# Kernel optimization log

Hardware: AMD Instinct MI355X
Metric: run time of the kernel (lower is better)

## Reference

```python
import jax, jax.numpy as jnp
import numpy as np

B, F, S = 2, 512, 1024
E = 4
I = 1024          # intermediate = 2 * features
K = 3             # conv kernel size
INIT_SCALE = 1.0
EPS = 1e-5
SLOPE = 0.02


def setup_inputs() -> dict:
    key = jax.random.key(0)
    k = jax.random.split(key, 6)
    inp = jax.random.normal(k[0], (B, F, S), jnp.float32)
    divisor = (jnp.arange(S, dtype=jnp.float32) + 1.0).reshape(1, 1, S)
    w0_gate = jax.random.normal(k[1], (E, F, 1), jnp.float32) * (F ** -0.5)
    w0 = jax.random.normal(k[2], (E, F, 3 * I), jnp.float32) * (F ** -0.5)
    w1 = jax.random.normal(k[3], (3 * I, I, K), jnp.float32) * ((I * K) ** -0.5)
    w2_gate = jax.random.normal(k[4], (E, I, 1), jnp.float32) * (I ** -0.5)
    w2 = jax.random.normal(k[5], (E, I, F), jnp.float32) * (I ** -0.5)
    return {"inp": inp, "divisor": divisor, "w0_gate": w0_gate, "w0": w0,
            "w1": w1, "w2_gate": w2_gate, "w2": w2}


def _norm(x):
    # channel norm over dim 1: subtract mean, divide by scaled L2 norm
    x = x - jnp.mean(x, axis=1, keepdims=True)
    n = jnp.sqrt(jnp.sum(x * x, axis=1, keepdims=True)) * (x.shape[1] ** -0.5)
    return x / (n + EPS)


def _moe(x, gate, w):
    # x: [B,F,S]; gate: [E,F,1]; w: [E,F,D]
    logits = jnp.einsum('bfs,ef->bes', x, gate[:, :, 0])          # [B,E,S]
    gates = jax.nn.softmax(logits, axis=1)
    idx = jnp.argmax(logits, axis=1)                              # [B,S]
    one_hot = jax.nn.one_hot(idx, w.shape[0], dtype=x.dtype)      # [B,S,E]
    # straight-through gumbel-style gate: hard one-hot fwd, soft grad
    gumbel = jnp.transpose(one_hot, (0, 2, 1)) - jax.lax.stop_gradient(gates) + gates  # [B,E,S]
    xs = jnp.transpose(x, (0, 2, 1))                              # [B,S,F]
    out = jnp.zeros((x.shape[0], x.shape[2], w.shape[2]), x.dtype)
    for e in range(w.shape[0]):  # small fixed expert count
        mask = one_hot[:, :, e][:, :, None]                       # [B,S,1]
        out = out + mask * ((xs * gumbel[:, e, :, None]) @ w[e])
    loss = jnp.sum(jnp.mean(gates, axis=(0, 2)) * jnp.mean(one_hot, axis=(0, 1)))
    return loss, jnp.transpose(out, (0, 2, 1))                    # [B,D,S]


def _conv1d(x, w, causal_pad):
    if causal_pad and w.shape[-1] > 1:
        x = jnp.pad(x, ((0, 0), (0, 0), (w.shape[-1] - 1, 0)))
    return jax.lax.conv_general_dilated(
        x, w, window_strides=(1,), padding='VALID',
        dimension_numbers=('NCH', 'OIH', 'NCH'), feature_group_count=1)


def reference(inp, divisor, w0_gate, w0, w1, w2_gate, w2):
    loss0, h = _moe(inp, w0_gate, w0)                 # [B,3I,S]
    depth, scale, shift = jnp.split(h, 3, axis=1)     # each [B,I,S]
    cum = jnp.cumsum(depth, axis=-1)
    h = jax.nn.leaky_relu(_norm(cum / divisor * scale + shift), SLOPE)
    h = _conv1d(h, w1, causal_pad=True)               # [B,3I,S]
    s0, s1, sh = jnp.split(h, 3, axis=1)
    h = jax.nn.leaky_relu(_norm(s0 * s1 + sh), SLOPE)
    loss1, out = _moe(h, w2_gate, w2)                 # [B,F,S]
    return out * INIT_SCALE, loss0 + loss1
```

## Files before the change

kernel.cpp:

```cpp
#include <hip/hip_runtime.h>
#include <hip/hip_bf16.h>

#define SDIM 1024

typedef float f32x4 __attribute__((ext_vector_type(4)));
typedef short short8 __attribute__((ext_vector_type(8)));

__device__ __forceinline__ unsigned short f2bf(float f) {
    __hip_bfloat16 h = __float2bfloat16(f);
    return *reinterpret_cast<unsigned short*>(&h);
}
__device__ __forceinline__ float bf2f(unsigned short u) {
    return __uint_as_float(((unsigned int)u) << 16);
}
__device__ __forceinline__ void gload_lds16(const unsigned short* g, unsigned short* l) {
    __builtin_amdgcn_global_load_lds((const __attribute__((address_space(1))) void*)g,
                                     (__attribute__((address_space(3))) void*)l, 16, 0, 0);
}

__device__ __forceinline__ void tr_split(
    const float* __restrict__ in, unsigned short* __restrict__ oh,
    unsigned short* __restrict__ ol, int R, int C, size_t sliceStride,
    int bx, int by, int slice, int tid, float (*t)[33])
{
    int c0 = bx * 32, r0 = by * 32;
    int cc = tid & 31, r8 = tid >> 5;
    const float* ip = in + slice * sliceStride;
    #pragma unroll
    for (int k = 0; k < 4; ++k) {
        int r = r8 + k * 8;
        t[r][cc] = ip[(size_t)(r0 + r) * C + c0 + cc];
    }
    __syncthreads();
    #pragma unroll
    for (int k = 0; k < 4; ++k) {
        int rr = r8 + k * 8;
        float v = t[cc][rr];
        unsigned short hi = f2bf(v);
        unsigned short lo = f2bf(v - bf2f(hi));
        size_t o = slice * sliceStride + (size_t)(c0 + rr) * R + r0 + cc;
        oh[o] = hi; ol[o] = lo;
    }
}

__global__ __launch_bounds__(256) void prep_kernel(
    const float* __restrict__ inp, const float* __restrict__ w0,
    const float* __restrict__ w1,
    unsigned short* __restrict__ xTh, unsigned short* __restrict__ xTl,
    unsigned short* __restrict__ w0Th, unsigned short* __restrict__ w0Tl,
    unsigned short* __restrict__ w1Th, unsigned short* __restrict__ w1Tl,
    const float* __restrict__ wg, int* __restrict__ idx, float* __restrict__ acc)
{
    __shared__ float t[32][33];
    __shared__ float wgs[4 * 512];
    __shared__ float part[32][4][9];
    __shared__ float la[8];
    int id = blockIdx.x;
    int tid = threadIdx.x;
    if (id < 1024) {
        int bx = id & 31, by = (id >> 5) & 15, slice = id >> 9;
        tr_split(inp, xTh, xTl, 512, 1024, (size_t)512 * 1024, bx, by, slice, tid, t);
    } else if (id < 7168) {
        int m = id - 1024;
        int bx = m % 96, by = (m / 96) & 15, slice = m / 1536;
        tr_split(w0, w0Th, w0Tl, 512, 3072, (size_t)512 * 3072, bx, by, slice, tid, t);
    } else if (id < 19456) {
        int tt = (id - 7168) * 256 + tid;
        int o = tt >> 10, i = tt & 1023;
        const float* p = w1 + (size_t)o * 3072 + i * 3;
        #pragma unroll
        for (int k = 0; k < 3; ++k) {
            float v = p[k];
            unsigned short hi = f2bf(v);
            unsigned short lo = f2bf(v - bf2f(hi));
            size_t off = (size_t)k * 3145728 + (size_t)o * 1024 + i;
            w1Th[off] = hi; w1Tl[off] = lo;
        }
    } else {
        if (tid < 8) la[tid] = 0.f;
        for (int l = tid; l < 2048; l += 256) wgs[l] = wg[l];
        __syncthreads();
        int t0 = (id - 19456) * 8;
        int b = t0 >> 10, s0 = t0 & 1023;
        int sl = tid & 7, fg = tid >> 3;
        float l0 = 0.f, l1 = 0.f, l2 = 0.f, l3 = 0.f;
        for (int f = fg; f < 512; f += 32) {
            float xv = inp[((size_t)b * 512 + f) * SDIM + s0 + sl];
            l0 += xv * wgs[f];
            l1 += xv * wgs[512 + f];
            l2 += xv * wgs[1024 + f];
            l3 += xv * wgs[1536 + f];
        }
        part[fg][0][sl] = l0; part[fg][1][sl] = l1;
        part[fg][2][sl] = l2; part[fg][3][sl] = l3;
        __syncthreads();
        for (int h = 16; h >= 1; h >>= 1) {
            if (fg < h) {
                #pragma unroll
                for (int e = 0; e < 4; ++e) part[fg][e][sl] += part[fg + h][e][sl];
            }
            __syncthreads();
        }
        if (fg == 0) {
            float L[4] = {part[0][0][sl], part[0][1][sl], part[0][2][sl], part[0][3][sl]};
            float m = fmaxf(fmaxf(L[0], L[1]), fmaxf(L[2], L[3]));
            float e0 = expf(L[0] - m), e1 = expf(L[1] - m), e2 = expf(L[2] - m), e3 = expf(L[3] - m);
            float inv = 1.0f / (e0 + e1 + e2 + e3);
            int best = 0; float bv = L[0];
            if (L[1] > bv) { bv = L[1]; best = 1; }
            if (L[2] > bv) { bv = L[2]; best = 2; }
            if (L[3] > bv) { bv = L[3]; best = 3; }
            idx[t0 + sl] = best;
            atomicAdd(&la[0], e0 * inv);
            atomicAdd(&la[1], e1 * inv);
            atomicAdd(&la[2], e2 * inv);
            atomicAdd(&la[3], e3 * inv);
            atomicAdd(&la[4 + best], 1.0f);
        }
        __syncthreads();
        if (tid < 8) atomicAdd(&acc[tid], la[tid]);
    }
}

__global__ __launch_bounds__(1024) void sort_kernel(
    const int* __restrict__ idx, int* __restrict__ perm, int* __restrict__ eSorted)
{
    int b = blockIdx.x;
    int tid = threadIdx.x;
    int lane = tid & 63, w = tid >> 6;
    int e = idx[(b << 10) + tid];
    __shared__ int wcnt[16][4];
    __shared__ int woff[16][4];
    int r = 0;
    unsigned long long lt = (1ull << lane) - 1ull;
    #pragma unroll
    for (int eo = 0; eo < 4; ++eo) {
        unsigned long long m = __ballot(e == eo);
        if (lane == 0) wcnt[w][eo] = __popcll(m);
        if (e == eo) r = __popcll(m & lt);
    }
    __syncthreads();
    if (tid == 0) {
        int baseAcc = 0;
        for (int eo = 0; eo < 4; ++eo)
            for (int ww = 0; ww < 16; ++ww) { woff[ww][eo] = baseAcc; baseAcc += wcnt[ww][eo]; }
    }
    __syncthreads();
    int pos = woff[w][e] + r;
    perm[(b << 10) + pos] = tid;
    eSorted[(b << 10) + pos] = e;
}

__global__ __launch_bounds__(768) void moe_split_kernel(
    const unsigned short* __restrict__ base, unsigned int XH, unsigned int XL,
    unsigned int WH, unsigned int WL,
    const int* __restrict__ perm, const int* __restrict__ eSorted,
    float* __restrict__ out)
{
    extern __shared__ unsigned short lds[];
    const int BUF = 40960;
    int id = blockIdx.x;
    int wg = (id & 7) * 32 + (id >> 3);
    int t0 = (wg & 7) * 256;
    int d0 = (wg >> 3) * 96;
    int b = t0 >> 10, s0 = t0 & 1023;
    int tid = threadIdx.x;
    int lane = tid & 63;
    int lm = lane & 15, q = lane >> 4;
    int wid = tid >> 6;
    int wm = (wid >> 2) * 32, wn = (wid & 3) * 64;

    int eLo = eSorted[(b << 10) + s0];
    int eHi = eSorted[(b << 10) + s0 + 255];

    unsigned int gofs[7];
    int lofs[7], doSeg[7];
    #pragma unroll
    for (int j = 0; j < 7; ++j) {
        int seg = wid + 12 * j;
        gofs[j] = 0; lofs[j] = 0; doSeg[j] = 0;
        if (seg < 80) {
            int row = seg * 16 + (lane >> 2);
            int slot = lane & 3;
            int c = slot ^ ((row >> 1) & 3);
            unsigned int src;
            int act = 1;
            if (row < 512) {
                int gr = (row < 256) ? row : row - 256;
                unsigned int hb = (row < 256) ? XH : XL;
                int tj = perm[(b << 10) + s0 + gr];
                src = hb + (unsigned int)(((b << 10) + tj) * 512) + c * 8;
            } else {
                int R = row - 512;
                unsigned int hb = WH;
                if (R >= 384) { R -= 384; hb = WL; }
                int e = R / 96, dl = R - e * 96;
                act = (e >= eLo && e <= eHi) ? 1 : 0;
                src = hb + (unsigned int)((e * 3072 + d0 + dl) * 512) + c * 8;
            }
            gofs[j] = src;
            lofs[j] = seg * 512 + lane * 8;
            doSeg[j] = act;
        }
    }

    int bofH[4];
    #pragma unroll
    for (int fn = 0; fn < 4; ++fn) {
        int row = wn + fn * 16 + lm;
        bofH[fn] = row * 32 + ((q ^ ((row >> 1) & 3)) << 3);
    }
    int aofH[4][2];
    #pragma unroll
    for (int e = 0; e < 4; ++e)
        #pragma unroll
        for (int fm = 0; fm < 2; ++fm) {
            int row = 512 + e * 96 + wm + fm * 16 + lm;
            aofH[e][fm] = row * 32 + ((q ^ ((row >> 1) & 3)) << 3);
        }

    int eidx[4], sv[4];
    #pragma unroll
    for (int fn = 0; fn < 4; ++fn) {
        int sl = (b << 10) + s0 + wn + fn * 16 + lm;
        eidx[fn] = eSorted[sl];
        sv[fn]   = perm[sl];
    }
    bool presF[4][4], presE[4];
    #pragma unroll
    for (int e = 0; e < 4; ++e) {
        presE[e] = false;
        #pragma unroll
        for (int fn = 0; fn < 4; ++fn) {
            presF[e][fn] = __any(eidx[fn] == e);
            presE[e] = presE[e] || presF[e][fn];
        }
    }

    f32x4 acc[2][4];
    #pragma unroll
    for (int fm = 0; fm < 2; ++fm)
        #pragma unroll
        for (int fn = 0; fn < 4; ++fn)
            acc[fm][fn] = (f32x4){0.f, 0.f, 0.f, 0.f};

    const short8 z = {0, 0, 0, 0, 0, 0, 0, 0};

    #pragma unroll
    for (int j = 0; j < 7; ++j)
        if (doSeg[j]) gload_lds16(base + gofs[j], lds + lofs[j]);

    int curOfs = 0;
    for (int f0 = 0; f0 < 512; f0 += 32) {
        __syncthreads();
        int nxtOfs = curOfs ^ BUF;
        if (f0 + 32 < 512) {
            #pragma unroll
            for (int j = 0; j < 7; ++j)
                if (doSeg[j]) gload_lds16(base + gofs[j] + f0 + 32, lds + nxtOfs + lofs[j]);
        }

        const unsigned short* lb = lds + curOfs;
        short8 bh[4], bl[4];
        #pragma unroll
        for (int fn = 0; fn < 4; ++fn) {
            bh[fn] = *(const short8*)(lb + bofH[fn]);
            bl[fn] = *(const short8*)(lb + bofH[fn] + 8192);
        }
        #pragma unroll
        for (int e = 0; e < 4; ++e) {
            if (presE[e]) {
                short8 ah[2], al[2];
                #pragma unroll
                for (int fm = 0; fm < 2; ++fm) {
                    ah[fm] = *(const short8*)(lb + aofH[e][fm]);
                    al[fm] = *(const short8*)(lb + aofH[e][fm] + 12288);
                }
                __builtin_amdgcn_s_setprio(1);
                #pragma unroll
                for (int fn = 0; fn < 4; ++fn) {
                    if (presF[e][fn]) {
                        short8 bmH = (eidx[fn] == e) ? bh[fn] : z;
                        short8 bmL = (eidx[fn] == e) ? bl[fn] : z;
                        #pragma unroll
                        for (int fm = 0; fm < 2; ++fm) {
                            acc[fm][fn] = __builtin_amdgcn_mfma_f32_16x16x32_bf16(ah[fm], bmH, acc[fm][fn], 0, 0, 0);
                            acc[fm][fn] = __builtin_amdgcn_mfma_f32_16x16x32_bf16(ah[fm], bmL, acc[fm][fn], 0, 0, 0);
                            acc[fm][fn] = __builtin_amdgcn_mfma_f32_16x16x32_bf16(al[fm], bmH, acc[fm][fn], 0, 0, 0);
                        }
                    }
                }
                __builtin_amdgcn_s_setprio(0);
            }
        }
        curOfs = nxtOfs;
    }

    #pragma unroll
    for (int fm = 0; fm < 2; ++fm)
        #pragma unroll
        for (int fn = 0; fn < 4; ++fn) {
            int d = d0 + wm + fm * 16 + q * 4;
            float* op = out + ((size_t)b * 3072 + d) * SDIM + sv[fn];
            #pragma unroll
            for (int r = 0; r < 4; ++r)
                op[(size_t)r * SDIM] = acc[fm][fn][r];
        }
}

__global__ __launch_bounds__(768) void conv_split_kernel(
    const unsigned short* __restrict__ base, unsigned int GH, unsigned int GL,
    unsigned int WH, unsigned int WL, unsigned int ZB, float* __restrict__ co)
{
    extern __shared__ unsigned short lds[];
    const int BUF = 35328;
    int id = blockIdx.x;
    int wg = (id & 7) * 32 + (id >> 3);
    int t0 = (wg & 7) * 256;
    int o0 = (wg >> 3) * 96;
    int b = t0 >> 10, s0 = t0 & 1023;
    int tid = threadIdx.x;
    int lane = tid & 63;
    int lm = lane & 15, q = lane >> 4;
    int wid = tid >> 6;
    int wm = (wid >> 2) * 32, wn = (wid & 3) * 64;

    unsigned int gofs[6];
    int lofs[6];
    int nseg = (wid < 9) ? 6 : 5;
    #pragma unroll
    for (int j = 0; j < 6; ++j) {
        int seg = wid + 12 * j;
        gofs[j] = ZB; lofs[j] = 0;
        if (seg < 69) {
            int row = seg * 16 + (lane >> 2);
            int slot = lane & 3;
            int c = slot ^ ((row >> 1) & 3);
            unsigned int src;
            if (row < 528) {
                int gr = (row < 264) ? row : row - 264;
                unsigned int hb = (row < 264) ? GH : GL;
                int s = s0 - 2 + gr;
                if (s < 0) src = ZB + c * 8;
                else { if (s > 1023) s = 1023;
                       src = hb + ((unsigned int)((b << 10) + s) << 10) + c * 8; }
            } else {
                int R = row - 528;
                unsigned int hb = WH;
                if (R >= 288) { R -= 288; hb = WL; }
                int k = R / 96, ol = R - k * 96;
                src = hb + (unsigned int)k * 3145728u + ((unsigned int)(o0 + ol) << 10) + c * 8;
            }
            gofs[j] = src;
            lofs[j] = seg * 512 + lane * 8;
        }
    }

    int aofH[3][2], aofL[3][2], bofH[3][4], bofL[3][4];
    #pragma unroll
    for (int k = 0; k < 3; ++k) {
        #pragma unroll
        for (int fm = 0; fm < 2; ++fm) {
            int R = k * 96 + wm + fm * 16 + lm;
            int rh = 528 + R, rl = 816 + R;
            aofH[k][fm] = rh * 32 + ((q ^ ((rh >> 1) & 3)) << 3);
            aofL[k][fm] = rl * 32 + ((q ^ ((rl >> 1) & 3)) << 3);
        }
        #pragma unroll
        for (int fn = 0; fn < 4; ++fn) {
            int rh = wn + fn * 16 + lm + k;
            int rl = rh + 264;
            bofH[k][fn] = rh * 32 + ((q ^ ((rh >> 1) & 3)) << 3);
            bofL[k][fn] = rl * 32 + ((q ^ ((rl >> 1) & 3)) << 3);
        }
    }

    f32x4 acc[2][4];
    #pragma unroll
    for (int fm = 0; fm < 2; ++fm)
        #pragma unroll
        for (int fn = 0; fn < 4; ++fn)
            acc[fm][fn] = (f32x4){0.f, 0.f, 0.f, 0.f};

    #pragma unroll
    for (int j = 0; j < 6; ++j)
        if (j < nseg) gload_lds16(base + gofs[j], lds + lofs[j]);

    int curOfs = 0;
    for (int i0 = 0; i0 < 1024; i0 += 32) {
        __syncthreads();
        int nxtOfs = curOfs ^ BUF;
        if (i0 + 32 < 1024) {
            #pragma unroll
            for (int j = 0; j < 6; ++j)
                if (j < nseg) gload_lds16(base + gofs[j] + i0 + 32, lds + nxtOfs + lofs[j]);
        }

        const unsigned short* lb = lds + curOfs;
        #pragma unroll
        for (int k = 0; k < 3; ++k) {
            short8 ah[2], al[2], bh[4], bl[4];
            #pragma unroll
            for (int fm = 0; fm < 2; ++fm) {
                ah[fm] = *(const short8*)(lb + aofH[k][fm]);
                al[fm] = *(const short8*)(lb + aofL[k][fm]);
            }
            #pragma unroll
            for (int fn = 0; fn < 4; ++fn) {
                bh[fn] = *(const short8*)(lb + bofH[k][fn]);
                bl[fn] = *(const short8*)(lb + bofL[k][fn]);
            }
            __builtin_amdgcn_s_setprio(1);
            #pragma unroll
            for (int fm = 0; fm < 2; ++fm)
                #pragma unroll
                for (int fn = 0; fn < 4; ++fn) {
                    acc[fm][fn] = __builtin_amdgcn_mfma_f32_16x16x32_bf16(ah[fm], bh[fn], acc[fm][fn], 0, 0, 0);
                    acc[fm][fn] = __builtin_amdgcn_mfma_f32_16x16x32_bf16(ah[fm], bl[fn], acc[fm][fn], 0, 0, 0);
                    acc[fm][fn] = __builtin_amdgcn_mfma_f32_16x16x32_bf16(al[fm], bh[fn], acc[fm][fn], 0, 0, 0);
                }
            __builtin_amdgcn_s_setprio(0);
        }
        curOfs = nxtOfs;
    }

    #pragma unroll
    for (int fm = 0; fm < 2; ++fm)
        #pragma unroll
        for (int fn = 0; fn < 4; ++fn) {
            int o = o0 + wm + fm * 16 + q * 4;
            int s = s0 + wn + fn * 16 + lm;
            float* op = co + ((size_t)b * 3072 + o) * SDIM + s;
            #pragma unroll
            for (int r = 0; r < 4; ++r)
                op[(size_t)r * SDIM] = acc[fm][fn][r];
        }
}

__global__ __launch_bounds__(256) void moe_kernel(
    const unsigned short* __restrict__ xT, const unsigned short* __restrict__ wT,
    const int* __restrict__ perm, const int* __restrict__ eSorted,
    float* __restrict__ out, int Fdim, int Ddim, const float* __restrict__ accv)
{
    if (blockIdx.x == 0 && threadIdx.x == 0) {
        float l = 0.f;
        #pragma unroll
        for (int e = 0; e < 4; ++e)
            l += accv[e] * accv[4 + e] + accv[8 + e] * accv[12 + e];
        out[2 * 512 * 1024] = l * (1.0f / (2048.0f * 2048.0f));
    }
    __shared__ unsigned short lds[384 * 32];
    int id = blockIdx.x;
    int chunk = gridDim.x >> 3;
    int wg = (id & 7) * chunk + (id >> 3);
    int t0 = (wg & 15) * 128;
    int d0 = (wg >> 4) * 64;
    int b = t0 >> 10, s0 = t0 & 1023;
    int tid = threadIdx.x;
    int lane = tid & 63, wid = tid >> 6;
    int lm = lane & 15, q = lane >> 4;
    int wm = (wid >> 1) * 32, wn = (wid & 1) * 64;

    int eLo = eSorted[(b << 10) + s0];
    int eHi = eSorted[(b << 10) + s0 + 127];

    const unsigned short* gsrc[6];
    int lofs[6], doSeg[6];
    #pragma unroll
    for (int j = 0; j < 6; ++j) {
        int seg = wid + 4 * j;
        int row = seg * 16 + (lane >> 2);
        int slot = lane & 3;
        int c = slot ^ ((row >> 1) & 3);
        int act = 1;
        const unsigned short* src;
        if (row < 128) {
            int tj = perm[(b << 10) + s0 + row];
            src = xT + (size_t)((b << 10) + tj) * Fdim + c * 8;
        } else {
            int R = row - 128;
            int e = R >> 6;
            act = (e >= eLo && e <= eHi) ? 1 : 0;
            src = wT + (size_t)(e * Ddim + d0 + (R & 63)) * Fdim + c * 8;
        }
        gsrc[j] = src; lofs[j] = seg * 512 + lane * 8; doSeg[j] = act;
    }

    int bof[4], aof[4][2];
    #pragma unroll
    for (int fn = 0; fn < 4; ++fn) {
        int row = wn + fn * 16 + lm;
        bof[fn] = row * 32 + ((q ^ ((row >> 1) & 3)) << 3);
    }
    #pragma unroll
    for (int e = 0; e < 4; ++e)
        #pragma unroll
        for (int fm = 0; fm < 2; ++fm) {
            int R = 128 + e * 64 + wm + fm * 16 + lm;
            aof[e][fm] = R * 32 + ((q ^ ((R >> 1) & 3)) << 3);
        }

    int eidx[4], sv[4];
    #pragma unroll
    for (int fn = 0; fn < 4; ++fn) {
        int sl = (b << 10) + s0 + wn + fn * 16 + lm;
        eidx[fn] = eSorted[sl];
        sv[fn]   = perm[sl];
    }
    bool presF[4][4], presE[4];
    #pragma unroll
    for (int e = 0; e < 4; ++e) {
        presE[e] = false;
        #pragma unroll
        for (int fn = 0; fn < 4; ++fn) {
            presF[e][fn] = __any(eidx[fn] == e);
            presE[e] = presE[e] || presF[e][fn];
        }
    }

    f32x4 acc[2][4];
    #pragma unroll
    for (int fm = 0; fm < 2; ++fm)
        #pragma unroll
        for (int fn = 0; fn < 4; ++fn)
            acc[fm][fn] = (f32x4){0.f, 0.f, 0.f, 0.f};

    const short8 z = {0, 0, 0, 0, 0, 0, 0, 0};

    for (int f0 = 0; f0 < Fdim; f0 += 32) {
        __syncthreads();
        #pragma unroll
        for (int j = 0; j < 6; ++j)
            if (doSeg[j]) gload_lds16(gsrc[j] + f0, lds + lofs[j]);
        __syncthreads();

        short8 bf[4];
        #pragma unroll
        for (int fn = 0; fn < 4; ++fn)
            bf[fn] = *(const short8*)(lds + bof[fn]);
        #pragma unroll
        for (int e = 0; e < 4; ++e) {
            if (presE[e]) {
                short8 af[2];
                #pragma unroll
                for (int fm = 0; fm < 2; ++fm)
                    af[fm] = *(const short8*)(lds + aof[e][fm]);
                #pragma unroll
                for (int fn = 0; fn < 4; ++fn) {
                    if (presF[e][fn]) {
                        short8 bm = (eidx[fn] == e) ? bf[fn] : z;
                        #pragma unroll
                        for (int fm = 0; fm < 2; ++fm)
                            acc[fm][fn] = __builtin_amdgcn_mfma_f32_16x16x32_bf16(af[fm], bm, acc[fm][fn], 0, 0, 0);
                    }
                }
            }
        }
    }

    #pragma unroll
    for (int fm = 0; fm < 2; ++fm)
        #pragma unroll
        for (int fn = 0; fn < 4; ++fn) {
            int d = d0 + wm + fm * 16 + q * 4;
            float* op = out + ((size_t)b * Ddim + d) * SDIM + sv[fn];
            #pragma unroll
            for (int r = 0; r < 4; ++r)
                op[(size_t)r * SDIM] = acc[fm][fn][r];
        }
}

__global__ __launch_bounds__(256) void cumsum_w2t_kernel(
    const float* __restrict__ h1, const float* __restrict__ divisor,
    float* __restrict__ y, const float* __restrict__ w2, unsigned short* __restrict__ w2T)
{
    __shared__ float tsh[32][33];
    __shared__ float wsum[4];
    int blk = blockIdx.x;
    int tid = threadIdx.x;
    if (blk >= 2048) {
        int m = blk - 2048;
        int bx = m & 15, by = (m >> 4) & 31, slice = m >> 9;
        int c0 = bx * 32, r0 = by * 32;
        int cc = tid & 31, r8 = tid >> 5;
        const float* ip = w2 + (size_t)slice * 524288;
        unsigned short* op = w2T + (size_t)slice * 524288;
        #pragma unroll
        for (int k = 0; k < 4; ++k) {
            int r = r8 + k * 8;
            tsh[r][cc] = ip[(size_t)(r0 + r) * 512 + c0 + cc];
        }
        __syncthreads();
        #pragma unroll
        for (int k = 0; k < 4; ++k) {
            int rr = r8 + k * 8;
            op[(size_t)(c0 + rr) * 1024 + r0 + cc] = f2bf(tsh[cc][rr]);
        }
        return;
    }
    int b = blk >> 10, i = blk & 1023;
    const float4* dp = (const float4*)(h1 + ((size_t)b * 3072 + i) * SDIM);
    const float4* sp = (const float4*)(h1 + ((size_t)b * 3072 + 1024 + i) * SDIM);
    const float4* hp = (const float4*)(h1 + ((size_t)b * 3072 + 2048 + i) * SDIM);
    float4 v = dp[tid];
    float c0 = v.x, c1 = c0 + v.y, c2 = c1 + v.z, c3 = c2 + v.w;
    int lane = tid & 63, w = tid >> 6;
    float sc = c3;
    #pragma unroll
    for (int off = 1; off < 64; off <<= 1) {
        float p = __shfl_up(sc, off);
        if (lane >= off) sc += p;
    }
    if (lane == 63) wsum[w] = sc;
    __syncthreads();
    float wbase = 0.f;
    #pragma unroll
    for (int ww = 0; ww < 4; ++ww)
        if (ww < w) wbase += wsum[ww];
    float base = wbase + sc - c3;
    float4 scv = sp[tid], sh = hp[tid];
    float4 dv = ((const float4*)divisor)[tid];
    float4 o;
    o.x = (base + c0) / dv.x * scv.x + sh.x;
    o.y = (base + c1) / dv.y * scv.y + sh.y;
    o.z = (base + c2) / dv.z * scv.z + sh.z;
    o.w = (base + c3) / dv.w * scv.w + sh.w;
    ((float4*)(y + ((size_t)b * 1024 + i) * SDIM))[tid] = o;
}

__global__ __launch_bounds__(256) void norm0_kernel(
    const float* __restrict__ g, unsigned short* __restrict__ oh,
    unsigned short* __restrict__ ol)
{
    int blk = blockIdx.x;
    int b = blk >> 7;
    int s0 = (blk & 127) * 8;
    int tid = threadIdx.x;
    int sg = tid & 7, grp = tid >> 3;
    int s = s0 + sg;
    const float* bp = g + ((size_t)b * 1024) * SDIM + s;
    float v[32];
    float sum = 0.f, ssq = 0.f;
    #pragma unroll
    for (int j = 0; j < 32; ++j) {
        float x = bp[(size_t)(grp * 32 + j) * SDIM];
        v[j] = x; sum += x; ssq += x * x;
    }
    __shared__ float rs[32][8], rq[32][8], stat[2][8];
    rs[grp][sg] = sum; rq[grp][sg] = ssq;
    __syncthreads();
    for (int h = 16; h >= 1; h >>= 1) {
        if (grp < h) { rs[grp][sg] += rs[grp + h][sg]; rq[grp][sg] += rq[grp + h][sg]; }
        __syncthreads();
    }
    if (grp == 0) {
        float S1 = rs[0][sg], S2 = rq[0][sg];
        float mean = S1 * (1.0f / 1024.0f);
        float ssc = fmaxf(S2 - 1024.0f * mean * mean, 0.0f);
        stat[0][sg] = mean;
        stat[1][sg] = 1.0f / (sqrtf(ssc) * (1.0f / 32.0f) + 1e-5f);
    }
    __syncthreads();
    float mean = stat[0][sg], inv = stat[1][sg];
    size_t tbase = (((size_t)b << 10) + s) * 1024 + grp * 32;
    #pragma unroll
    for (int j0 = 0; j0 < 32; j0 += 4) {
        unsigned short uh[4], ul[4];
        #pragma unroll
        for (int jj = 0; jj < 4; ++jj) {
            float o = (v[j0 + jj] - mean) * inv;
            o = (o >= 0.f) ? o : 0.02f * o;
            uh[jj] = f2bf(o);
            ul[jj] = f2bf(o - bf2f(uh[jj]));
        }
        *(ushort4*)(oh + tbase + j0) = (ushort4){uh[0], uh[1], uh[2], uh[3]};
        *(ushort4*)(ol + tbase + j0) = (ushort4){ul[0], ul[1], ul[2], ul[3]};
    }
}

__global__ __launch_bounds__(256) void normgate_kernel(
    const float* __restrict__ h1, const float* __restrict__ wg,
    unsigned short* __restrict__ outT, int* __restrict__ idx, float* __restrict__ acc)
{
    int blk = blockIdx.x;
    int b = blk >> 7;
    int s0 = (blk & 127) * 8;
    int tid = threadIdx.x;
    int sg = tid & 7, grp = tid >> 3;
    int s = s0 + sg;
    const float* bp = h1 + ((size_t)b * 3072) * SDIM + s;
    float v[32];
    float sum = 0.f, ssq = 0.f;
    #pragma unroll
    for (int j = 0; j < 32; ++j) {
        int i = grp * 32 + j;
        float a  = bp[(size_t)i * SDIM];
        float m2 = bp[(size_t)(1024 + i) * SDIM];
        float d2 = bp[(size_t)(2048 + i) * SDIM];
        float x = a * m2 + d2;
        v[j] = x; sum += x; ssq += x * x;
    }
    __shared__ float rs[32][8], rq[32][8], stat[2][8];
    rs[grp][sg] = sum; rq[grp][sg] = ssq;
    __syncthreads();
    for (int h = 16; h >= 1; h >>= 1) {
        if (grp < h) { rs[grp][sg] += rs[grp + h][sg]; rq[grp][sg] += rq[grp + h][sg]; }
        __syncthreads();
    }
    if (grp == 0) {
        float S1 = rs[0][sg], S2 = rq[0][sg];
        float mean = S1 * (1.0f / 1024.0f);
        float ssc = fmaxf(S2 - 1024.0f * mean * mean, 0.0f);
        stat[0][sg] = mean;
        stat[1][sg] = 1.0f / (sqrtf(ssc) * (1.0f / 32.0f) + 1e-5f);
    }
    __syncthreads();
    float mean = stat[0][sg], inv = stat[1][sg];
    float l0 = 0.f, l1 = 0.f, l2 = 0.f, l3 = 0.f;
    size_t tbase = (((size_t)b << 10) + s) * 1024 + grp * 32;
    #pragma unroll
    for (int j0 = 0; j0 < 32; j0 += 4) {
        unsigned short u[4];
        #pragma unroll
        for (int jj = 0; jj < 4; ++jj) {
            int i = grp * 32 + j0 + jj;
            float o = (v[j0 + jj] - mean) * inv;
            o = (o >= 0.f) ? o : 0.02f * o;
            u[jj] = f2bf(o);
            l0 += o * wg[i];
            l1 += o * wg[1024 + i];
            l2 += o * wg[2048 + i];
            l3 += o * wg[3072 + i];
        }
        *(ushort4*)(outT + tbase + j0) = (ushort4){u[0], u[1], u[2], u[3]};
    }
    __shared__ float pl[4][32][8];
    __shared__ float la[8];
    pl[0][grp][sg] = l0; pl[1][grp][sg] = l1;
    pl[2][grp][sg] = l2; pl[3][grp][sg] = l3;
    if (tid < 8) la[tid] = 0.f;
    __syncthreads();
    for (int h = 16; h >= 1; h >>= 1) {
        if (grp < h) {
            #pragma unroll
            for (int e = 0; e < 4; ++e) pl[e][grp][sg] += pl[e][grp + h][sg];
        }
        __syncthreads();
    }
    if (grp == 0) {
        float L[4] = {pl[0][0][sg], pl[1][0][sg], pl[2][0][sg], pl[3][0][sg]};
        float m = fmaxf(fmaxf(L[0], L[1]), fmaxf(L[2], L[3]));
        float e0 = expf(L[0] - m), e1 = expf(L[1] - m), e2 = expf(L[2] - m), e3 = expf(L[3] - m);
        float invs = 1.0f / (e0 + e1 + e2 + e3);
        int best = 0; float bv = L[0];
        if (L[1] > bv) { bv = L[1]; best = 1; }
        if (L[2] > bv) { bv = L[2]; best = 2; }
        if (L[3] > bv) { bv = L[3]; best = 3; }
        idx[(b << 10) + s] = best;
        atomicAdd(&la[0], e0 * invs);
        atomicAdd(&la[1], e1 * invs);
        atomicAdd(&la[2], e2 * invs);
        atomicAdd(&la[3], e3 * invs);
        atomicAdd(&la[4 + best], 1.0f);
    }
    __syncthreads();
    if (tid < 8) atomicAdd(&acc[8 + tid], la[tid]);
}

extern "C" void kernel_launch(void* const* d_in, const int* in_sizes, int n_in,
                              void* d_out, int out_size, void* d_ws, size_t ws_size,
                              hipStream_t stream) {
    const float* inp     = (const float*)d_in[0];
    const float* divisor = (const float*)d_in[1];
    const float* w0_gate = (const float*)d_in[2];
    const float* w0      = (const float*)d_in[3];
    const float* w1      = (const float*)d_in[4];
    const float* w2_gate = (const float*)d_in[5];
    const float* w2      = (const float*)d_in[6];
    float* out = (float*)d_out;
    (void)in_sizes; (void)n_in; (void)out_size; (void)ws_size;

    char* ws = (char*)d_ws;
    const unsigned short* base = (const unsigned short*)ws;

    float* h1            = (float*)(ws + 0);
    float* g             = (float*)(ws + 25165824);
    unsigned short* gT1h = (unsigned short*)(ws + 33554432);
    unsigned short* gT1l = (unsigned short*)(ws + 37748736);
    unsigned short* w1Th = (unsigned short*)(ws + 41943040);
    unsigned short* w1Tl = (unsigned short*)(ws + 60817408);
    unsigned short* xTh  = (unsigned short*)(ws + 79691776);
    unsigned short* xTl  = (unsigned short*)(ws + 81788928);
    unsigned short* w0Th = (unsigned short*)(ws + 83886080);
    unsigned short* w0Tl = (unsigned short*)(ws + 96468992);
    unsigned short* gT2  = (unsigned short*)(ws + 79691776);
    unsigned short* w2T  = (unsigned short*)(ws + 83886080);
    int* idx1            = (int*)(ws + 109051904);
    int* idx2            = (int*)(ws + 109060096);
    float* acc           = (float*)(ws + 109068288);
    int* perm1           = (int*)(ws + 109076480);
    int* eSort1          = (int*)(ws + 109084672);
    int* perm2           = (int*)(ws + 109092864);
    int* eSort2          = (int*)(ws + 109101056);
    float* zbuf          = (float*)(ws + 109109248);

    const unsigned int GT1H = 16777216u, GT1L = 18874368u;
    const unsigned int W1TH = 20971520u, W1TL = 30408704u;
    const unsigned int XTH  = 39845888u, XTL  = 40894464u;
    const unsigned int W0TH = 41943040u, W0TL = 48234496u;
    const unsigned int ZB   = 54554624u;

    hipMemsetAsync(acc, 0, 64, stream);
    hipMemsetAsync(zbuf, 0, 4096, stream);

    prep_kernel<<<19712, 256, 0, stream>>>(inp, w0, w1, xTh, xTl, w0Th, w0Tl,
                                           w1Th, w1Tl, w0_gate, idx1, acc);

    sort_kernel<<<2, 1024, 0, stream>>>(idx1, perm1, eSort1);
    moe_split_kernel<<<256, 768, 163840, stream>>>(base, XTH, XTL, W0TH, W0TL, perm1, eSort1, h1);

    cumsum_w2t_kernel<<<4096, 256, 0, stream>>>(h1, divisor, g, w2, w2T);
    norm0_kernel<<<256, 256, 0, stream>>>(g, gT1h, gT1l);
    conv_split_kernel<<<256, 768, 141312, stream>>>(base, GT1H, GT1L, W1TH, W1TL, ZB, h1);
    normgate_kernel<<<256, 256, 0, stream>>>(h1, w2_gate, gT2, idx2, acc);

    sort_kernel<<<2, 1024, 0, stream>>>(idx2, perm2, eSort2);
    moe_kernel<<<128, 256, 0, stream>>>(gT2, w2T, perm2, eSort2, out, 1024, 512, acc);
}
```

Before: 239.3 us.

## Store conv output transposed and rework conv wave tiling to 16 waves

The conv kernel now runs 16 waves per block, each computing a 48x32 tile instead of 12 waves on 32x64 tiles, and the LDS load segments are redistributed across the extra waves. Its output is written in a [B*S, 3072] transposed layout as contiguous float4 stores instead of strided scalar stores. The normgate kernel then reads rows with float4 vector loads instead of column-strided scalar loads. This is meant to cut uncoalesced global traffic in both kernels and raise wave-level parallelism, at the cost of a different MFMA A/B reuse ratio and possible register pressure at 1024 threads.

After: 232.6 us, median of 2. 1.03x faster.

```diff
diff --git a/kernel.cpp b/kernel.cpp
--- a/kernel.cpp
+++ b/kernel.cpp
@@ -308,9 +308,9 @@
         }
 }
 
-__global__ __launch_bounds__(768) void conv_split_kernel(
+__global__ __launch_bounds__(1024) void conv_split_kernel(
     const unsigned short* __restrict__ base, unsigned int GH, unsigned int GL,
-    unsigned int WH, unsigned int WL, unsigned int ZB, float* __restrict__ co)
+    unsigned int WH, unsigned int WL, unsigned int ZB, float* __restrict__ h1T)
 {
     extern __shared__ unsigned short lds[];
     const int BUF = 35328;
@@ -323,14 +323,14 @@
     int lane = tid & 63;
     int lm = lane & 15, q = lane >> 4;
     int wid = tid >> 6;
-    int wm = (wid >> 2) * 32, wn = (wid & 3) * 64;
-
-    unsigned int gofs[6];
-    int lofs[6];
-    int nseg = (wid < 9) ? 6 : 5;
-    #pragma unroll
-    for (int j = 0; j < 6; ++j) {
-        int seg = wid + 12 * j;
+    int wm = (wid >> 3) * 48, wn = (wid & 7) * 32;
+
+    unsigned int gofs[5];
+    int lofs[5];
+    int nseg = (wid < 5) ? 5 : 4;
+    #pragma unroll
+    for (int j = 0; j < 5; ++j) {
+        int seg = wid + 16 * j;
         gofs[j] = ZB; lofs[j] = 0;
         if (seg < 69) {
             int row = seg * 16 + (lane >> 2);
@@ -356,18 +356,18 @@
         }
     }
 
-    int aofH[3][2], aofL[3][2], bofH[3][4], bofL[3][4];
+    int aofH[3][3], aofL[3][3], bofH[3][2], bofL[3][2];
     #pragma unroll
     for (int k = 0; k < 3; ++k) {
         #pragma unroll
-        for (int fm = 0; fm < 2; ++fm) {
+        for (int fm = 0; fm < 3; ++fm) {
             int R = k * 96 + wm + fm * 16 + lm;
             int rh = 528 + R, rl = 816 + R;
             aofH[k][fm] = rh * 32 + ((q ^ ((rh >> 1) & 3)) << 3);
             aofL[k][fm] = rl * 32 + ((q ^ ((rl >> 1) & 3)) << 3);
         }
         #pragma unroll
-        for (int fn = 0; fn < 4; ++fn) {
+        for (int fn = 0; fn < 2; ++fn) {
             int rh = wn + fn * 16 + lm + k;
             int rl = rh + 264;
             bofH[k][fn] = rh * 32 + ((q ^ ((rh >> 1) & 3)) << 3);
@@ -375,15 +375,15 @@
         }
     }
 
-    f32x4 acc[2][4];
-    #pragma unroll
-    for (int fm = 0; fm < 2; ++fm)
-        #pragma unroll
-        for (int fn = 0; fn < 4; ++fn)
+    f32x4 acc[3][2];
+    #pragma unroll
+    for (int fm = 0; fm < 3; ++fm)
+        #pragma unroll
+        for (int fn = 0; fn < 2; ++fn)
             acc[fm][fn] = (f32x4){0.f, 0.f, 0.f, 0.f};
 
     #pragma unroll
-    for (int j = 0; j < 6; ++j)
+    for (int j = 0; j < 5; ++j)
         if (j < nseg) gload_lds16(base + gofs[j], lds + lofs[j]);
 
     int curOfs = 0;
@@ -392,29 +392,29 @@
         int nxtOfs = curOfs ^ BUF;
         if (i0 + 32 < 1024) {
             #pragma unroll
-            for (int j = 0; j < 6; ++j)
+            for (int j = 0; j < 5; ++j)
                 if (j < nseg) gload_lds16(base + gofs[j] + i0 + 32, lds + nxtOfs + lofs[j]);
         }
 
         const unsigned short* lb = lds + curOfs;
         #pragma unroll
         for (int k = 0; k < 3; ++k) {
-            short8 ah[2], al[2], bh[4], bl[4];
+            short8 ah[3], al[3], bh[2], bl[2];
             #pragma unroll
-            for (int fm = 0; fm < 2; ++fm) {
+            for (int fm = 0; fm < 3; ++fm) {
                 ah[fm] = *(const short8*)(lb + aofH[k][fm]);
                 al[fm] = *(const short8*)(lb + aofL[k][fm]);
             }
             #pragma unroll
-            for (int fn = 0; fn < 4; ++fn) {
+            for (int fn = 0; fn < 2; ++fn) {
                 bh[fn] = *(const short8*)(lb + bofH[k][fn]);
                 bl[fn] = *(const short8*)(lb + bofL[k][fn]);
             }
             __builtin_amdgcn_s_setprio(1);
             #pragma unroll
-            for (int fm = 0; fm < 2; ++fm)
+            for (int fm = 0; fm < 3; ++fm)
                 #pragma unroll
-                for (int fn = 0; fn < 4; ++fn) {
+                for (int fn = 0; fn < 2; ++fn) {
                     acc[fm][fn] = __builtin_amdgcn_mfma_f32_16x16x32_bf16(ah[fm], bh[fn], acc[fm][fn], 0, 0, 0);
                     acc[fm][fn] = __builtin_amdgcn_mfma_f32_16x16x32_bf16(ah[fm], bl[fn], acc[fm][fn], 0, 0, 0);
                     acc[fm][fn] = __builtin_amdgcn_mfma_f32_16x16x32_bf16(al[fm], bh[fn], acc[fm][fn], 0, 0, 0);
@@ -425,15 +425,12 @@
     }
 
     #pragma unroll
-    for (int fm = 0; fm < 2; ++fm)
-        #pragma unroll
-        for (int fn = 0; fn < 4; ++fn) {
+    for (int fm = 0; fm < 3; ++fm)
+        #pragma unroll
+        for (int fn = 0; fn < 2; ++fn) {
             int o = o0 + wm + fm * 16 + q * 4;
             int s = s0 + wn + fn * 16 + lm;
-            float* op = co + ((size_t)b * 3072 + o) * SDIM + s;
-            #pragma unroll
-            for (int r = 0; r < 4; ++r)
-                op[(size_t)r * SDIM] = acc[fm][fn][r];
+            *(f32x4*)(h1T + ((size_t)((b << 10) + s)) * 3072 + o) = acc[fm][fn];
         }
 }
 
@@ -679,7 +676,7 @@
 }
 
 __global__ __launch_bounds__(256) void normgate_kernel(
-    const float* __restrict__ h1, const float* __restrict__ wg,
+    const float* __restrict__ h1T, const float* __restrict__ wg,
     unsigned short* __restrict__ outT, int* __restrict__ idx, float* __restrict__ acc)
 {
     int blk = blockIdx.x;
@@ -688,17 +685,22 @@
     int tid = threadIdx.x;
     int sg = tid & 7, grp = tid >> 3;
     int s = s0 + sg;
-    const float* bp = h1 + ((size_t)b * 3072) * SDIM + s;
+    const float* row = h1T + ((size_t)((b << 10) + s)) * 3072;
     float v[32];
     float sum = 0.f, ssq = 0.f;
     #pragma unroll
-    for (int j = 0; j < 32; ++j) {
-        int i = grp * 32 + j;
-        float a  = bp[(size_t)i * SDIM];
-        float m2 = bp[(size_t)(1024 + i) * SDIM];
-        float d2 = bp[(size_t)(2048 + i) * SDIM];
-        float x = a * m2 + d2;
-        v[j] = x; sum += x; ssq += x * x;
+    for (int j0 = 0; j0 < 32; j0 += 4) {
+        int i = grp * 32 + j0;
+        float4 av = *(const float4*)(row + i);
+        float4 mv = *(const float4*)(row + 1024 + i);
+        float4 dv = *(const float4*)(row + 2048 + i);
+        float x0 = av.x * mv.x + dv.x;
+        float x1 = av.y * mv.y + dv.y;
+        float x2 = av.z * mv.z + dv.z;
+        float x3 = av.w * mv.w + dv.w;
+        v[j0] = x0; v[j0 + 1] = x1; v[j0 + 2] = x2; v[j0 + 3] = x3;
+        sum += x0 + x1 + x2 + x3;
+        ssq += x0 * x0 + x1 * x1 + x2 * x2 + x3 * x3;
     }
     __shared__ float rs[32][8], rq[32][8], stat[2][8];
     rs[grp][sg] = sum; rq[grp][sg] = ssq;
@@ -821,7 +823,7 @@
 
     cumsum_w2t_kernel<<<4096, 256, 0, stream>>>(h1, divisor, g, w2, w2T);
     norm0_kernel<<<256, 256, 0, stream>>>(g, gT1h, gT1l);
-    conv_split_kernel<<<256, 768, 141312, stream>>>(base, GT1H, GT1L, W1TH, W1TL, ZB, h1);
+    conv_split_kernel<<<256, 1024, 141312, stream>>>(base, GT1H, GT1L, W1TH, W1TL, ZB, h1);
     normgate_kernel<<<256, 256, 0, stream>>>(h1, w2_gate, gT2, idx2, acc);
 
     sort_kernel<<<2, 1024, 0, stream>>>(idx2, perm2, eSort2);
```
